# Optimization experiments

Measured on AMD Instinct MI355X. Metric: run time of the kernel, lower is better.

## Reference

```python
import jax, jax.numpy as jnp
import numpy as np


def _split_feature(x, ns):
    # channel-last split: [b,h,w,c] -> [b*ns*ns, h/ns, w/ns, c]
    b, h, w, c = x.shape
    hn, wn = h // ns, w // ns
    return x.reshape(b, ns, hn, ns, wn, c).transpose(0, 1, 3, 2, 4, 5).reshape(b * ns * ns, hn, wn, c)


def _merge_splits(x, ns):
    # inverse of _split_feature: [b*ns*ns, h, w, c] -> [b, ns*h, ns*w, c]
    b, h, w, c = x.shape
    nb = b // (ns * ns)
    return x.reshape(nb, ns, ns, h, w, c).transpose(0, 1, 3, 2, 4, 5).reshape(nb, ns * h, ns * w, c)


def _gen_shift_window_attn_mask(h, w, ns):
    # numpy replica of _unimatch_generate_shift_window_attn_mask
    wsh, wsw = h // ns, w // ns
    ssh, ssw = wsh // 2, wsw // 2
    img = np.zeros((1, h, w, 1), dtype=np.float32)
    cnt = 0
    for hs in (slice(0, -wsh), slice(-wsh, -ssh), slice(-ssh, None)):
        for ws in (slice(0, -wsw), slice(-wsw, -ssw), slice(-ssw, None)):
            img[:, hs, ws, :] = cnt
            cnt += 1
    win = img.reshape(1, ns, wsh, ns, wsw, 1).transpose(0, 1, 3, 2, 4, 5).reshape(ns * ns, wsh * wsw)
    am = win[:, None, :] - win[:, :, None]
    return np.where(am != 0, np.float32(-100.0), np.float32(0.0)).astype(np.float32)


def setup_inputs() -> dict:
    key = jax.random.key(0)
    B, H, W, C, NS = 8, 96, 128, 128, 4
    kq, kk, kv = jax.random.split(key, 3)
    q = jax.random.normal(kq, (B, H * W, C), jnp.float32)
    k = jax.random.normal(kk, (B, H * W, C), jnp.float32)
    v = jax.random.normal(kv, (B, H * W, C), jnp.float32)
    attn_mask = jnp.asarray(_gen_shift_window_attn_mask(H, W, NS))  # [NS*NS, n, n]
    return {"q": q, "k": k, "v": v, "attn_mask": attn_mask,
            "num_splits": NS, "with_shift": 1, "h": H, "w": W}


def reference(q, k, v, attn_mask, num_splits, with_shift, h, w):
    b, _, c = q.shape
    ns = num_splits
    wsh, wsw = h // ns, w // ns
    n = wsh * wsw
    bn = b * ns * ns
    q = q.reshape(b, h, w, c)
    k = k.reshape(b, h, w, c)
    v = v.reshape(b, h, w, c)
    if with_shift:
        sh, sw = wsh // 2, wsw // 2
        q = jnp.roll(q, (-sh, -sw), axis=(1, 2))
        k = jnp.roll(k, (-sh, -sw), axis=(1, 2))
        v = jnp.roll(v, (-sh, -sw), axis=(1, 2))
    qf = _split_feature(q, ns).reshape(bn, n, c)
    kf = _split_feature(k, ns).reshape(bn, n, c)
    vf = _split_feature(v, ns).reshape(bn, n, c)
    scale = jnp.asarray(c, qf.dtype) ** 0.5
    scores = jnp.einsum('bnc,bmc->bnm', qf, kf) / scale  # [bn, n, n]
    if with_shift:
        scores = scores + jnp.tile(attn_mask, (b, 1, 1))
    attn = jax.nn.softmax(scores, axis=-1)
    out = jnp.einsum('bnm,bmc->bnc', attn, vf)
    out = _merge_splits(out.reshape(bn, wsh, wsw, c), ns)  # [b, h, w, c]
    if with_shift:
        out = jnp.roll(out, (sh, sw), axis=(1, 2))
    return out.reshape(b, h * w, c)
```

## Files before the change

kernel.cpp:

```cpp
#include <hip/hip_runtime.h>

#define H 96
#define W 128
#define C 128
#define WSH 24
#define WSW 32
#define NTOK 768
#define SH 12
#define SW 16
#define KT 32
#define NKT 24
#define PSTR 40
#define TILE_USH 8192
#define WS_NEED (128L * NKT * TILE_USH * 2)

typedef __attribute__((ext_vector_type(8))) short short8;
typedef __attribute__((ext_vector_type(4))) float floatx4;

__device__ inline unsigned short f2bf(float f) {
  union { float f; unsigned u; } un; un.f = f;
  unsigned r = un.u + 0x7FFF + ((un.u >> 16) & 1);
  return (unsigned short)(r >> 16);
}

__device__ inline int tok_off(int tok, int wh, int ww) {
  int r = tok >> 5;
  int cc = tok & 31;
  int y = wh * WSH + r + SH; if (y >= H) y -= H;
  int x = ww * WSW + cc + SW; if (x >= W) x -= W;
  return y * W + x;
}

__global__ __launch_bounds__(256) void prep_kernel(const float* __restrict__ k,
                                                   const float* __restrict__ v,
                                                   unsigned short* __restrict__ ws) {
  __shared__ unsigned short Vlds[KT][136];
  const int bid = blockIdx.x;
  const int w = bid / NKT;
  const int kt = bid - w * NKT;
  const int batch = w >> 4, win = w & 15;
  const int wh = win >> 2, ww = win & 3;
  int y = wh * WSH + kt + SH; if (y >= H) y -= H;

  const int t = threadIdx.x;
  const int key = t >> 3;
  const int j = t & 7;
  const int c0 = j * 16;
  int x = ww * WSW + key + SW; if (x >= W) x -= W;
  const long src = ((long)batch * H * W + (long)y * W + x) * C + c0;
  unsigned short* tile = ws + (long)bid * TILE_USH;

  {
    const float* kp = k + src;
    short8 s0, s1;
#pragma unroll
    for (int i = 0; i < 2; ++i) {
      floatx4 a = *(const floatx4*)(kp + i * 8);
      floatx4 b = *(const floatx4*)(kp + i * 8 + 4);
      s0[i*4+0] = (short)f2bf(a[0]); s0[i*4+1] = (short)f2bf(a[1]);
      s0[i*4+2] = (short)f2bf(a[2]); s0[i*4+3] = (short)f2bf(a[3]);
      s1[i*4+0] = (short)f2bf(b[0]); s1[i*4+1] = (short)f2bf(b[1]);
      s1[i*4+2] = (short)f2bf(b[2]); s1[i*4+3] = (short)f2bf(b[3]);
    }
    short8 o0, o1;
    o0[0]=s0[0]; o0[1]=s0[1]; o0[2]=s0[2]; o0[3]=s0[3]; o0[4]=s1[0]; o0[5]=s1[1]; o0[6]=s1[2]; o0[7]=s1[3];
    o1[0]=s0[4]; o1[1]=s0[5]; o1[2]=s0[6]; o1[3]=s0[7]; o1[4]=s1[4]; o1[5]=s1[5]; o1[6]=s1[6]; o1[7]=s1[7];
    const int kc = j >> 1;
    const int q2 = (j & 1) * 2;
    unsigned short* kout = tile + kc * 1024 + key * 32 + q2 * 8;
    *(short8*)(kout) = o0;
    *(short8*)(kout + 8) = o1;
  }
  {
    const float* vp = v + src;
#pragma unroll
    for (int i = 0; i < 4; ++i) {
      floatx4 a = *(const floatx4*)(vp + i * 4);
      Vlds[key][c0 + i*4 + 0] = f2bf(a[0]);
      Vlds[key][c0 + i*4 + 1] = f2bf(a[1]);
      Vlds[key][c0 + i*4 + 2] = f2bf(a[2]);
      Vlds[key][c0 + i*4 + 3] = f2bf(a[3]);
    }
  }
  __syncthreads();
  {
    const int cb = t >> 5;
    const int rem = t & 31;
    const int col = rem >> 1, qh = rem & 1;
    const int ch = cb * 16 + col;
#pragma unroll
    for (int qs = 0; qs < 2; ++qs) {
      const int quad = qh * 2 + qs;
      short8 o;
#pragma unroll
      for (int i = 0; i < 8; ++i)
        o[i] = (short)Vlds[(i & 1) * 16 + quad * 4 + (i >> 1)][ch];
      *(short8*)(tile + 4096 + cb * 512 + (col * 4 + quad) * 8) = o;
    }
  }
}

__global__ __launch_bounds__(128, 1) void attn_main(const float* __restrict__ q,
                                                    const unsigned short* __restrict__ ws,
                                                    float* __restrict__ out) {
  __shared__ unsigned short Ps[2][6][16 * PSTR];

  const int bid = blockIdx.x;
  const int x8 = bid & 7;
  const int i = bid >> 3;
  const int w = x8 * 16 + (i & 15);
  const int qb = i >> 4;
  const int batch = w >> 4, win = w & 15;
  const int wh = win >> 2, ww = win & 3;

  const int tid = threadIdx.x;
  const int wave = tid >> 6, lane = tid & 63;
  const int col = lane & 15, quad = lane >> 4;
  const long bbase = (long)batch * (H * W * C);
  const int qbase = qb * 192 + wave * 96;
  const int loff = (col * 4 + quad) * 8;

  short8 qfrag[6][4];
#pragma unroll
  for (int s = 0; s < 6; ++s) {
    const int qtok = qbase + s * 16 + col;
    const float* qp = q + bbase + (long)tok_off(qtok, wh, ww) * C + quad * 8;
#pragma unroll
    for (int kc = 0; kc < 4; ++kc) {
      floatx4 a = *(const floatx4*)(qp + kc * 32);
      floatx4 b = *(const floatx4*)(qp + kc * 32 + 4);
      short8 v8;
      v8[0]=(short)f2bf(a[0]); v8[1]=(short)f2bf(a[1]); v8[2]=(short)f2bf(a[2]); v8[3]=(short)f2bf(a[3]);
      v8[4]=(short)f2bf(b[0]); v8[5]=(short)f2bf(b[1]); v8[6]=(short)f2bf(b[2]); v8[7]=(short)f2bf(b[3]);
      qfrag[s][kc] = v8;
    }
  }

  int qreg[6];
#pragma unroll
  for (int s = 0; s < 6; ++s) {
    int rr_s = (qbase >> 5) + (s >> 1);
    int qh = (wh == 3) ? ((rr_s >= SH) ? 2 : 1) : 0;
    int qw = (ww == 3) ? ((s & 1) ? 2 : 1) : 0;
    qreg[s] = qh * 3 + qw;
  }
  const int cw0 = (ww == 3) ? 1 : 0, cw1 = (ww == 3) ? 2 : 0;
  const float MNEG = -144.2695041f;
  const float SC2 = 0.12751739f;

  floatx4 oacc[6][8];
#pragma unroll
  for (int s = 0; s < 6; ++s)
#pragma unroll
    for (int cb = 0; cb < 8; ++cb) oacc[s][cb] = (floatx4){0.f, 0.f, 0.f, 0.f};
  float lsum[6][4];
#pragma unroll
  for (int s = 0; s < 6; ++s)
#pragma unroll
    for (int r = 0; r < 4; ++r) lsum[s][r] = 0.f;

  const unsigned short* wsw_ = ws + (long)w * (NKT * TILE_USH);

  short8 kf0[4], kf1[4];
  auto load_k = [&](int kt) {
    const unsigned short* tk = wsw_ + ((long)kt << 13);
#pragma unroll
    for (int kc = 0; kc < 4; ++kc) {
      kf0[kc] = *(const short8*)(tk + kc * 1024 + loff);
      kf1[kc] = *(const short8*)(tk + kc * 1024 + 512 + loff);
    }
  };
  load_k(0);

  for (int kt = 0; kt < NKT; ++kt) {
    const unsigned short* tv = wsw_ + ((long)kt << 13) + 4096;
    short8 vf[8];
#pragma unroll
    for (int cb = 0; cb < 8; ++cb) vf[cb] = *(const short8*)(tv + cb * 512 + loff);

    const int khb = (wh == 3) ? ((kt >= SH) ? 6 : 3) : 0;
    const int kr0 = khb + cw0, kr1 = khb + cw1;

#pragma unroll
    for (int s = 0; s < 6; ++s) {
      floatx4 a0 = (floatx4){0.f, 0.f, 0.f, 0.f};
      floatx4 a1 = (floatx4){0.f, 0.f, 0.f, 0.f};
#pragma unroll
      for (int kc = 0; kc < 4; ++kc) {
        a0 = __builtin_amdgcn_mfma_f32_16x16x32_bf16(qfrag[s][kc], kf0[kc], a0, 0, 0, 0);
        a1 = __builtin_amdgcn_mfma_f32_16x16x32_bf16(qfrag[s][kc], kf1[kc], a1, 0, 0, 0);
      }
      const float m0 = (qreg[s] == kr0) ? 0.f : MNEG;
      const float m1 = (qreg[s] == kr1) ? 0.f : MNEG;
#pragma unroll
      for (int r = 0; r < 4; ++r) {
        float p0 = __builtin_amdgcn_exp2f(fmaf(a0[r], SC2, m0));
        float p1 = __builtin_amdgcn_exp2f(fmaf(a1[r], SC2, m1));
        lsum[s][r] += p0 + p1;
        unsigned pk = (unsigned)f2bf(p0) | ((unsigned)f2bf(p1) << 16);
        *(unsigned*)&Ps[wave][s][(quad * 4 + r) * PSTR + 2 * col] = pk;
      }
    }

    if (kt + 1 < NKT) load_k(kt + 1);

#pragma unroll
    for (int s = 0; s < 6; ++s) {
      short8 pf = *(const short8*)&Ps[wave][s][col * PSTR + quad * 8];
#pragma unroll
      for (int cb = 0; cb < 8; ++cb)
        oacc[s][cb] = __builtin_amdgcn_mfma_f32_16x16x32_bf16(pf, vf[cb], oacc[s][cb], 0, 0, 0);
    }
  }

#pragma unroll
  for (int s = 0; s < 6; ++s)
#pragma unroll
    for (int r = 0; r < 4; ++r) {
      float l = lsum[s][r];
      l += __shfl_xor(l, 1); l += __shfl_xor(l, 2);
      l += __shfl_xor(l, 4); l += __shfl_xor(l, 8);
      float inv = 1.0f / l;
      int tok = qbase + s * 16 + quad * 4 + r;
      float* op = out + bbase + (long)tok_off(tok, wh, ww) * C + col;
#pragma unroll
      for (int cb = 0; cb < 8; ++cb) op[cb * 16] = oacc[s][cb][r] * inv;
    }
}

#define KSTRF 136
#define VSTRF 40
#define PSTRF 40
__global__ __launch_bounds__(256, 2) void attn_fallback(
    const float* __restrict__ q, const float* __restrict__ k,
    const float* __restrict__ v, const float* __restrict__ mask,
    float* __restrict__ out) {
  __shared__ unsigned short Ks[KT * KSTRF];
  __shared__ unsigned short Vtl[C * VSTRF];
  __shared__ unsigned short Psf[4][16 * PSTRF];
  const int qtile = blockIdx.x;
  const int beta  = blockIdx.y;
  const int batch = beta >> 4;
  const int win   = beta & 15;
  const int wh = win >> 2, ww = win & 3;
  const int tid = threadIdx.x;
  const int wave = tid >> 6, lane = tid & 63;
  const int col = lane & 15, quad = lane >> 4;
  const long bbase = (long)batch * (H * W * C);
  const int qtok = qtile * 64 + wave * 16 + col;
  const float* qp = q + bbase + (long)tok_off(qtok, wh, ww) * C + quad * 8;
  short8 qfrag[4];
#pragma unroll
  for (int kc = 0; kc < 4; ++kc) {
    floatx4 a = *(const floatx4*)(qp + kc * 32);
    floatx4 b = *(const floatx4*)(qp + kc * 32 + 4);
    short8 s;
    s[0]=f2bf(a[0]); s[1]=f2bf(a[1]); s[2]=f2bf(a[2]); s[3]=f2bf(a[3]);
    s[4]=f2bf(b[0]); s[5]=f2bf(b[1]); s[6]=f2bf(b[2]); s[7]=f2bf(b[3]);
    qfrag[kc] = s;
  }
  floatx4 oacc[8];
#pragma unroll
  for (int i = 0; i < 8; ++i) oacc[i] = (floatx4){0.f,0.f,0.f,0.f};
  float mrow[4], lrow[4];
#pragma unroll
  for (int r = 0; r < 4; ++r) { mrow[r] = -1e30f; lrow[r] = 0.f; }
  const int skey = tid >> 3;
  const int sch  = (tid & 7) * 4;
  const float invscale = 0.088388347648318447f;
  const float* maskw = mask + (long)win * (NTOK * NTOK);
  const int qrow_m = qtile * 64 + wave * 16 + quad * 4;
  for (int kt = 0; kt < NKT; ++kt) {
    const int ktok0 = kt * KT;
    const long srow = bbase + (long)tok_off(ktok0 + skey, wh, ww) * C;
    const float* kp = k + srow;
    const float* vp = v + srow;
    __syncthreads();
#pragma unroll
    for (int j = 0; j < 4; ++j) {
      floatx4 f = *(const floatx4*)(kp + sch + j * 32);
      unsigned lo = (unsigned)f2bf(f[0]) | ((unsigned)f2bf(f[1]) << 16);
      unsigned hi = (unsigned)f2bf(f[2]) | ((unsigned)f2bf(f[3]) << 16);
      *(uint2*)&Ks[skey * KSTRF + sch + j * 32] = make_uint2(lo, hi);
    }
#pragma unroll
    for (int j = 0; j < 4; ++j) {
      floatx4 f = *(const floatx4*)(vp + sch + j * 32);
      int chb = sch + j * 32;
      Vtl[(chb + 0) * VSTRF + skey] = f2bf(f[0]);
      Vtl[(chb + 1) * VSTRF + skey] = f2bf(f[1]);
      Vtl[(chb + 2) * VSTRF + skey] = f2bf(f[2]);
      Vtl[(chb + 3) * VSTRF + skey] = f2bf(f[3]);
    }
    __syncthreads();
    floatx4 s0 = (floatx4){0.f,0.f,0.f,0.f};
    floatx4 s1 = (floatx4){0.f,0.f,0.f,0.f};
#pragma unroll
    for (int kc = 0; kc < 4; ++kc) {
      short8 k0 = *(const short8*)&Ks[col * KSTRF + kc * 32 + quad * 8];
      short8 k1 = *(const short8*)&Ks[(col + 16) * KSTRF + kc * 32 + quad * 8];
      s0 = __builtin_amdgcn_mfma_f32_16x16x32_bf16(qfrag[kc], k0, s0, 0, 0, 0);
      s1 = __builtin_amdgcn_mfma_f32_16x16x32_bf16(qfrag[kc], k1, s1, 0, 0, 0);
    }
    float mk0[4], mk1[4];
    const float* mp = maskw + (long)qrow_m * NTOK + ktok0 + col;
#pragma unroll
    for (int r = 0; r < 4; ++r) { mk0[r] = mp[r * NTOK]; mk1[r] = mp[r * NTOK + 16]; }
#pragma unroll
    for (int r = 0; r < 4; ++r) {
      float a0 = s0[r] * invscale + mk0[r];
      float a1 = s1[r] * invscale + mk1[r];
      float mx = fmaxf(a0, a1);
      mx = fmaxf(mx, __shfl_xor(mx, 1)); mx = fmaxf(mx, __shfl_xor(mx, 2));
      mx = fmaxf(mx, __shfl_xor(mx, 4)); mx = fmaxf(mx, __shfl_xor(mx, 8));
      float mnew = fmaxf(mrow[r], mx);
      float alpha = __expf(mrow[r] - mnew);
      float p0 = __expf(a0 - mnew);
      float p1 = __expf(a1 - mnew);
      float rs = p0 + p1;
      rs += __shfl_xor(rs, 1); rs += __shfl_xor(rs, 2);
      rs += __shfl_xor(rs, 4); rs += __shfl_xor(rs, 8);
      lrow[r] = lrow[r] * alpha + rs;
      mrow[r] = mnew;
#pragma unroll
      for (int cb = 0; cb < 8; ++cb) oacc[cb][r] *= alpha;
      Psf[wave][(quad * 4 + r) * PSTRF + col]      = f2bf(p0);
      Psf[wave][(quad * 4 + r) * PSTRF + 16 + col] = f2bf(p1);
    }
    __syncthreads();
    short8 pf = *(const short8*)&Psf[wave][col * PSTRF + quad * 8];
#pragma unroll
    for (int cb = 0; cb < 8; ++cb) {
      short8 vf = *(const short8*)&Vtl[(cb * 16 + col) * VSTRF + quad * 8];
      oacc[cb] = __builtin_amdgcn_mfma_f32_16x16x32_bf16(pf, vf, oacc[cb], 0, 0, 0);
    }
  }
#pragma unroll
  for (int r = 0; r < 4; ++r) {
    float inv_l = 1.0f / lrow[r];
    int tok = qtile * 64 + wave * 16 + quad * 4 + r;
    float* op = out + bbase + (long)tok_off(tok, wh, ww) * C + col;
#pragma unroll
    for (int cb = 0; cb < 8; ++cb) op[cb * 16] = oacc[cb][r] * inv_l;
  }
}

extern "C" void kernel_launch(void* const* d_in, const int* in_sizes, int n_in,
                              void* d_out, int out_size, void* d_ws, size_t ws_size,
                              hipStream_t stream) {
  const float* q    = (const float*)d_in[0];
  const float* k    = (const float*)d_in[1];
  const float* v    = (const float*)d_in[2];
  const float* mask = (const float*)d_in[3];
  float* out = (float*)d_out;
  if (ws_size >= (size_t)WS_NEED) {
    prep_kernel<<<128 * NKT, 256, 0, stream>>>(k, v, (unsigned short*)d_ws);
    attn_main<<<512, 128, 0, stream>>>(q, (const unsigned short*)d_ws, out);
  } else {
    attn_fallback<<<dim3(12, 128), dim3(256), 0, stream>>>(q, k, v, mask, out);
  }
}
```

Measured before the change: 248.2 us.

## Share K/V tiles across 8 waves via double-buffered LDS async staging

The attention kernel moves from 128-thread blocks (2 waves, 96 query rows each) to 512-thread blocks (8 waves, 48 rows each). Each block covers half a window, and K/V tiles are staged once per block into double-buffered LDS with global_load_lds, instead of every wave reading the tiles from global memory. This cuts redundant global/L2 traffic for K/V and lowers per-wave register pressure. In exchange it adds a block-wide __syncthreads per key tile and launches only 256 blocks, which may leave some CUs underused.

```diff
diff --git a/kernel.cpp b/kernel.cpp
--- a/kernel.cpp
+++ b/kernel.cpp
@@ -100,16 +100,17 @@
   }
 }
 
-__global__ __launch_bounds__(128, 1) void attn_main(const float* __restrict__ q,
-                                                    const unsigned short* __restrict__ ws,
-                                                    float* __restrict__ out) {
-  __shared__ unsigned short Ps[2][6][16 * PSTR];
+__global__ __launch_bounds__(512) void attn_main(const float* __restrict__ q,
+                                                 const unsigned short* __restrict__ ws,
+                                                 float* __restrict__ out) {
+  __shared__ unsigned short stage[2][TILE_USH];
+  __shared__ unsigned short Ps[8][3][16 * PSTR];
 
   const int bid = blockIdx.x;
   const int x8 = bid & 7;
-  const int i = bid >> 3;
-  const int w = x8 * 16 + (i & 15);
-  const int qb = i >> 4;
+  const int j = bid >> 3;
+  const int w = x8 * 16 + (j & 15);
+  const int qhalf = j >> 4;
   const int batch = w >> 4, win = w & 15;
   const int wh = win >> 2, ww = win & 3;
 
@@ -117,12 +118,12 @@
   const int wave = tid >> 6, lane = tid & 63;
   const int col = lane & 15, quad = lane >> 4;
   const long bbase = (long)batch * (H * W * C);
-  const int qbase = qb * 192 + wave * 96;
+  const int qbase = qhalf * 384 + wave * 48;
   const int loff = (col * 4 + quad) * 8;
 
-  short8 qfrag[6][4];
-#pragma unroll
-  for (int s = 0; s < 6; ++s) {
+  short8 qfrag[3][4];
+#pragma unroll
+  for (int s = 0; s < 3; ++s) {
     const int qtok = qbase + s * 16 + col;
     const float* qp = q + bbase + (long)tok_off(qtok, wh, ww) * C + quad * 8;
 #pragma unroll
@@ -136,53 +137,66 @@
     }
   }
 
-  int qreg[6];
-#pragma unroll
-  for (int s = 0; s < 6; ++s) {
-    int rr_s = (qbase >> 5) + (s >> 1);
-    int qh = (wh == 3) ? ((rr_s >= SH) ? 2 : 1) : 0;
-    int qw = (ww == 3) ? ((s & 1) ? 2 : 1) : 0;
+  int qreg[3];
+#pragma unroll
+  for (int s = 0; s < 3; ++s) {
+    const int base_s = qbase + s * 16;
+    const int rr = base_s >> 5;
+    const int colhalf = (base_s >> 4) & 1;
+    int qh = (wh == 3) ? ((rr >= SH) ? 2 : 1) : 0;
+    int qw = (ww == 3) ? (colhalf ? 2 : 1) : 0;
     qreg[s] = qh * 3 + qw;
   }
   const int cw0 = (ww == 3) ? 1 : 0, cw1 = (ww == 3) ? 2 : 0;
   const float MNEG = -144.2695041f;
   const float SC2 = 0.12751739f;
 
-  floatx4 oacc[6][8];
-#pragma unroll
-  for (int s = 0; s < 6; ++s)
+  floatx4 oacc[3][8];
+#pragma unroll
+  for (int s = 0; s < 3; ++s)
 #pragma unroll
     for (int cb = 0; cb < 8; ++cb) oacc[s][cb] = (floatx4){0.f, 0.f, 0.f, 0.f};
-  float lsum[6][4];
-#pragma unroll
-  for (int s = 0; s < 6; ++s)
+  float lsum[3][4];
+#pragma unroll
+  for (int s = 0; s < 3; ++s)
 #pragma unroll
     for (int r = 0; r < 4; ++r) lsum[s][r] = 0.f;
 
   const unsigned short* wsw_ = ws + (long)w * (NKT * TILE_USH);
 
-  short8 kf0[4], kf1[4];
-  auto load_k = [&](int kt) {
-    const unsigned short* tk = wsw_ + ((long)kt << 13);
+  auto stage_issue = [&](int kt, int buf) {
+    const unsigned short* gt = wsw_ + ((long)kt << 13);
+    auto lds3 = (__attribute__((address_space(3))) char*)&stage[buf][0];
+#pragma unroll
+    for (int jj = 0; jj < 2; ++jj) {
+      __builtin_amdgcn_global_load_lds(
+          (const __attribute__((address_space(1))) unsigned int*)(gt + (jj * 512 + tid) * 8),
+          (__attribute__((address_space(3))) unsigned int*)(lds3 + (jj * 512 + wave * 64) * 16),
+          16, 0, 0);
+    }
+  };
+
+  stage_issue(0, 0);
+  for (int kt = 0; kt < NKT; ++kt) {
+    const int cur = kt & 1;
+    __syncthreads();
+    if (kt + 1 < NKT) stage_issue(kt + 1, cur ^ 1);
+
+    const unsigned short* Kt = &stage[cur][0];
+    const unsigned short* Vt = &stage[cur][4096];
+
+    short8 kf0[4], kf1[4];
 #pragma unroll
     for (int kc = 0; kc < 4; ++kc) {
-      kf0[kc] = *(const short8*)(tk + kc * 1024 + loff);
-      kf1[kc] = *(const short8*)(tk + kc * 1024 + 512 + loff);
-    }
-  };
-  load_k(0);
-
-  for (int kt = 0; kt < NKT; ++kt) {
-    const unsigned short* tv = wsw_ + ((long)kt << 13) + 4096;
-    short8 vf[8];
-#pragma unroll
-    for (int cb = 0; cb < 8; ++cb) vf[cb] = *(const short8*)(tv + cb * 512 + loff);
+      kf0[kc] = *(const short8*)&Kt[kc * 1024 + loff];
+      kf1[kc] = *(const short8*)&Kt[kc * 1024 + 512 + loff];
+    }
 
     const int khb = (wh == 3) ? ((kt >= SH) ? 6 : 3) : 0;
     const int kr0 = khb + cw0, kr1 = khb + cw1;
 
 #pragma unroll
-    for (int s = 0; s < 6; ++s) {
+    for (int s = 0; s < 3; ++s) {
       floatx4 a0 = (floatx4){0.f, 0.f, 0.f, 0.f};
       floatx4 a1 = (floatx4){0.f, 0.f, 0.f, 0.f};
 #pragma unroll
@@ -202,19 +216,20 @@
       }
     }
 
-    if (kt + 1 < NKT) load_k(kt + 1);
-
-#pragma unroll
-    for (int s = 0; s < 6; ++s) {
-      short8 pf = *(const short8*)&Ps[wave][s][col * PSTR + quad * 8];
-#pragma unroll
-      for (int cb = 0; cb < 8; ++cb)
-        oacc[s][cb] = __builtin_amdgcn_mfma_f32_16x16x32_bf16(pf, vf[cb], oacc[s][cb], 0, 0, 0);
-    }
-  }
-
-#pragma unroll
-  for (int s = 0; s < 6; ++s)
+    short8 pf0 = *(const short8*)&Ps[wave][0][col * PSTR + quad * 8];
+    short8 pf1 = *(const short8*)&Ps[wave][1][col * PSTR + quad * 8];
+    short8 pf2 = *(const short8*)&Ps[wave][2][col * PSTR + quad * 8];
+#pragma unroll
+    for (int cb = 0; cb < 8; ++cb) {
+      short8 vf = *(const short8*)&Vt[cb * 512 + loff];
+      oacc[0][cb] = __builtin_amdgcn_mfma_f32_16x16x32_bf16(pf0, vf, oacc[0][cb], 0, 0, 0);
+      oacc[1][cb] = __builtin_amdgcn_mfma_f32_16x16x32_bf16(pf1, vf, oacc[1][cb], 0, 0, 0);
+      oacc[2][cb] = __builtin_amdgcn_mfma_f32_16x16x32_bf16(pf2, vf, oacc[2][cb], 0, 0, 0);
+    }
+  }
+
+#pragma unroll
+  for (int s = 0; s < 3; ++s)
 #pragma unroll
     for (int r = 0; r < 4; ++r) {
       float l = lsum[s][r];
@@ -355,7 +370,7 @@
   float* out = (float*)d_out;
   if (ws_size >= (size_t)WS_NEED) {
     prep_kernel<<<128 * NKT, 256, 0, stream>>>(k, v, (unsigned short*)d_ws);
-    attn_main<<<512, 128, 0, stream>>>(q, (const unsigned short*)d_ws, out);
+    attn_main<<<256, 512, 0, stream>>>(q, (const unsigned short*)d_ws, out);
   } else {
     attn_fallback<<<dim3(12, 128), dim3(256), 0, stream>>>(q, k, v, mask, out);
   }
```

New measurement: 249.3 us. Within noise of the previous version (+0.5%).
